# Kernel optimization log

Hardware: AMD Instinct MI355X
Metric: run time of the kernel (lower is better)

## Reference

```python
import jax, jax.numpy as jnp
import numpy as np


def setup_inputs() -> dict:
    key = jax.random.key(0)
    k0, k1, k2, k3, k4, k5 = jax.random.split(key, 6)
    B, V, Fin, K, Fout = 8, 49152, 64, 3, 64
    nnz = V * 8  # ~8 neighbors per vertex (HEALPix sphere graph)
    std = (2.0 / (Fin * K)) ** 0.5  # Kaiming-normal as in reset_parameters
    inputs = jax.random.normal(k0, (B, V, Fin), jnp.float32)
    weight = jax.random.normal(k1, (Fin, K, Fout), jnp.float32) * std
    bias = jax.random.normal(k2, (Fout,), jnp.float32) * 0.05
    lap_rows = jax.random.randint(k3, (nnz,), 0, V, jnp.int32)
    lap_cols = jax.random.randint(k4, (nnz,), 0, V, jnp.int32)
    lap_vals = jax.random.normal(k5, (nnz,), jnp.float32) * 0.1
    return {"inputs": inputs, "weight": weight, "bias": bias,
            "lap_rows": lap_rows, "lap_cols": lap_cols, "lap_vals": lap_vals}


def reference(inputs, weight, bias, lap_rows, lap_cols, lap_vals):
    B, V, Fin = inputs.shape
    _, K, Fout = weight.shape

    def spmm(x):  # sparse Laplacian (COO) @ dense [V, Fin*B]
        return jax.ops.segment_sum(lap_vals[:, None] * x[lap_cols], lap_rows,
                                   num_segments=V)

    # x0: [V, Fin*B], matching torch's permute(1,2,0).view(V, Fin*B)
    x0 = inputs.transpose(1, 2, 0).reshape(V, Fin * B)
    xs = [x0]
    if K > 1:
        x1 = spmm(x0)
        xs.append(x1)
    for _ in range(2, K):
        x2 = 2.0 * spmm(x1) - x0  # Chebyshev recurrence
        xs.append(x2)
        x0, x1 = x1, x2
    x = jnp.stack(xs)                                    # [K, V, Fin*B]
    x = x.reshape(K, V, Fin, B).transpose(3, 1, 2, 0)    # [B, V, Fin, K]
    x = x.reshape(B * V, Fin * K)
    out = x @ weight.reshape(Fin * K, Fout)              # dense GEMM
    return out.reshape(B, V, Fout) + bias
```

## Files before the change

kernel.cpp:

```cpp
#include <hip/hip_runtime.h>
#include <stdint.h>

#define B_   8
#define V_   49152
#define M_   (B_ * V_)

typedef unsigned short ushort_t;
typedef __attribute__((ext_vector_type(8))) short short8;
typedef __attribute__((ext_vector_type(4))) float float4v;

__device__ __forceinline__ float bf2f_lo(unsigned int pk) {
    union { unsigned int u; float f; } x; x.u = pk << 16; return x.f;
}
__device__ __forceinline__ float bf2f_hi(unsigned int pk) {
    union { unsigned int u; float f; } x; x.u = pk & 0xffff0000u; return x.f;
}
__device__ __forceinline__ ushort_t f2bf(float f) {
    union { unsigned int u; float f; } x; x.f = f;
    unsigned int u = x.u;
    unsigned int r = u + 0x7fffu + ((u >> 16) & 1u);
    return (ushort_t)(r >> 16);
}
__device__ __forceinline__ unsigned int pack2(float a, float b) {
    return ((unsigned int)f2bf(b) << 16) | (unsigned int)f2bf(a);
}
__device__ __forceinline__ void fma8(float* acc, float w, const uint4& p) {
    const unsigned int* u = (const unsigned int*)&p;
    #pragma unroll
    for (int i = 0; i < 4; i++) {
        acc[2 * i]     += w * bf2f_lo(u[i]);
        acc[2 * i + 1] += w * bf2f_hi(u[i]);
    }
}

__global__ void fill_sentinel(float* out, int n) {
    int i = blockIdx.x * blockDim.x + threadIdx.x;
    if (i < n) out[i] = 9999.0f;
}

#define PREP_B 3072
__global__ __launch_bounds__(256) void k1_fused(const float* __restrict__ inp,
                                                ushort_t* __restrict__ x0t,
                                                const int* __restrict__ rows, int nnz,
                                                int* __restrict__ counts,
                                                const float* __restrict__ wgt,
                                                ushort_t* __restrict__ wBf, int hb) {
    int bid = blockIdx.x;
    int t = threadIdx.x;
    if (bid < PREP_B) {
        int idx = bid * 256 + t;
        int f4 = idx & 15, v = idx >> 4;
        #pragma unroll
        for (int b = 0; b < 8; b++) {
            float4 d = *(const float4*)(inp + ((size_t)b * V_ + v) * 64 + f4 * 4);
            uint2 o = make_uint2(pack2(d.x, d.y), pack2(d.z, d.w));
            *(uint2*)(x0t + ((size_t)v * 8 + b) * 64 + f4 * 4) = o;
        }
    } else if (bid < PREP_B + hb) {
        int i = (bid - PREP_B) * 256 + t;
        if (i < nnz) atomicAdd(&counts[rows[i]], 1);
    } else {
        int idx = (bid - PREP_B - hb) * 256 + t;
        int j = idx & 7, lane = (idx >> 3) & 63, ntc = (idx >> 9) & 3, kb = idx >> 11;
        int k = kb * 32 + (lane >> 4) * 8 + j;
        int kc = k >> 6, fi = k & 63;
        int fo = ntc * 16 + (lane & 15);
        float w;
        if (kc == 0)      w = wgt[(fi * 3 + 0) * 64 + fo] - wgt[(fi * 3 + 2) * 64 + fo];
        else if (kc == 1) w = wgt[(fi * 3 + 1) * 64 + fo];
        else              w = 2.0f * wgt[(fi * 3 + 2) * 64 + fo];
        wBf[idx] = f2bf(w);
    }
}

__global__ __launch_bounds__(1024) void scan_kernel(const int* __restrict__ counts,
                                                    int* __restrict__ offsets) {
    __shared__ int s[1024];
    int t = threadIdx.x;
    int4 c[12];
    int sum = 0;
    #pragma unroll
    for (int j = 0; j < 12; j++) {
        int4 q = ((const int4*)counts)[t * 12 + j];
        q.x = (q.x + 3) & ~3; q.y = (q.y + 3) & ~3;
        q.z = (q.z + 3) & ~3; q.w = (q.w + 3) & ~3;
        c[j] = q;
        sum += q.x + q.y + q.z + q.w;
    }
    s[t] = sum;
    __syncthreads();
    for (int off = 1; off < 1024; off <<= 1) {
        int v = (t >= off) ? s[t - off] : 0;
        __syncthreads();
        s[t] += v;
        __syncthreads();
    }
    int run = (t == 0) ? 0 : s[t - 1];
    #pragma unroll
    for (int j = 0; j < 12; j++) {
        int4 o;
        o.x = run; run += c[j].x;
        o.y = run; run += c[j].y;
        o.z = run; run += c[j].z;
        o.w = run; run += c[j].w;
        ((int4*)offsets)[t * 12 + j] = o;
    }
    if (t == 1023) offsets[V_] = run;
}

__global__ void bucket_kernel(const int* __restrict__ rows, const int* __restrict__ cols,
                              const float* __restrict__ vals, int nnz,
                              const int* __restrict__ offsets, int* __restrict__ cursor,
                              uint2* __restrict__ e_cv) {
    int i = blockIdx.x * blockDim.x + threadIdx.x;
    if (i >= nnz) return;
    int r = rows[i];
    int p = offsets[r] + atomicAdd(&cursor[r], 1);
    e_cv[p] = make_uint2((unsigned int)cols[i], __float_as_uint(vals[i]));
}

__device__ __forceinline__ void gather16(const ushort_t* __restrict__ srcbf,
                                         const uint2* __restrict__ e_cv,
                                         int beg, int end, float* acc) {
    for (int e = beg; e < end; e += 4) {
        uint4 E0 = *(const uint4*)(e_cv + e);
        uint4 E1 = *(const uint4*)(e_cv + e + 2);
        float w0 = __uint_as_float(E0.y), w1 = __uint_as_float(E0.w);
        float w2 = __uint_as_float(E1.y), w3 = __uint_as_float(E1.w);
        const ushort_t* p0 = srcbf + ((size_t)E0.x * 512);
        const ushort_t* p1 = srcbf + ((size_t)E0.z * 512);
        const ushort_t* p2 = srcbf + ((size_t)E1.x * 512);
        const ushort_t* p3 = srcbf + ((size_t)E1.z * 512);
        uint4 a0 = *(const uint4*)p0, b0 = *(const uint4*)(p0 + 8);
        uint4 a1 = *(const uint4*)p1, b1 = *(const uint4*)(p1 + 8);
        uint4 a2 = *(const uint4*)p2, b2 = *(const uint4*)(p2 + 8);
        uint4 a3 = *(const uint4*)p3, b3 = *(const uint4*)(p3 + 8);
        fma8(acc, w0, a0); fma8(acc + 8, w0, b0);
        fma8(acc, w1, a1); fma8(acc + 8, w1, b1);
        fma8(acc, w2, a2); fma8(acc + 8, w2, b2);
        fma8(acc, w3, a3); fma8(acc + 8, w3, b3);
    }
}

__global__ __launch_bounds__(256) void spmm1_kernel(const ushort_t* __restrict__ x0t,
                                                    const int* __restrict__ offsets,
                                                    const uint2* __restrict__ e_cv,
                                                    ushort_t* __restrict__ x1) {
    int t = threadIdx.x;
    int vi = t >> 5, b = (t >> 2) & 7, f8 = t & 3;
    int v = blockIdx.x * 8 + vi;
    float acc[16];
    #pragma unroll
    for (int i = 0; i < 16; i++) acc[i] = 0.f;
    gather16(x0t + b * 64 + f8 * 16, e_cv, offsets[v], offsets[v + 1], acc);
    unsigned int opk[8];
    #pragma unroll
    for (int i = 0; i < 8; i++) opk[i] = pack2(acc[2 * i], acc[2 * i + 1]);
    ushort_t* dst = x1 + ((size_t)v * 8 + b) * 64 + f8 * 16;
    *(uint4*)dst       = make_uint4(opk[0], opk[1], opk[2], opk[3]);
    *(uint4*)(dst + 8) = make_uint4(opk[4], opk[5], opk[6], opk[7]);
}

__global__ __launch_bounds__(256) void spmm2_gemm(const ushort_t* __restrict__ x0t,
                                                  const ushort_t* __restrict__ x1,
                                                  const int* __restrict__ offsets,
                                                  const uint2* __restrict__ e_cv,
                                                  const ushort_t* __restrict__ wBf,
                                                  const float* __restrict__ bias,
                                                  float* __restrict__ out) {
    __shared__ ushort_t sh[64 * 72];
    int t = threadIdx.x;
    int lane = t & 63, wv = t >> 6;
    int quad = lane >> 4, col = lane & 15;
    int v0 = blockIdx.x * 8;
    int m0 = v0 * 8 + wv * 16;

    size_t arow = (size_t)(m0 + col) * 64 + quad * 8;
    short8 A0[2], A1[2];
    A0[0] = *(const short8*)(x0t + arow);
    A0[1] = *(const short8*)(x0t + arow + 32);
    A1[0] = *(const short8*)(x1 + arow);
    A1[1] = *(const short8*)(x1 + arow + 32);

    int vi = t >> 5, b = (t >> 2) & 7, f8 = t & 3;
    int v = v0 + vi;
    float acc[16];
    #pragma unroll
    for (int i = 0; i < 16; i++) acc[i] = 0.f;
    gather16(x1 + b * 64 + f8 * 16, e_cv, offsets[v], offsets[v + 1], acc);

    unsigned int opk[8];
    #pragma unroll
    for (int i = 0; i < 8; i++) opk[i] = pack2(acc[2 * i], acc[2 * i + 1]);
    int mg = vi * 8 + b;
    ushort_t* dst = sh + mg * 72 + f8 * 16;
    *(uint4*)dst       = make_uint4(opk[0], opk[1], opk[2], opk[3]);
    *(uint4*)(dst + 8) = make_uint4(opk[4], opk[5], opk[6], opk[7]);
    __syncthreads();

    short8 Bf[6][4];
    #pragma unroll
    for (int kb = 0; kb < 6; kb++)
        #pragma unroll
        for (int ntc = 0; ntc < 4; ntc++)
            Bf[kb][ntc] = *(const short8*)(wBf + ((size_t)((kb * 4 + ntc) * 64 + lane)) * 8);

    float bv[4];
    #pragma unroll
    for (int ntc = 0; ntc < 4; ntc++) bv[ntc] = bias[ntc * 16 + col];

    float4v accm[4];
    #pragma unroll
    for (int ntc = 0; ntc < 4; ntc++) accm[ntc] = (float4v){0.f, 0.f, 0.f, 0.f};

    #pragma unroll
    for (int p = 0; p < 2; p++) {
        #pragma unroll
        for (int ntc = 0; ntc < 4; ntc++)
            accm[ntc] = __builtin_amdgcn_mfma_f32_16x16x32_bf16(A0[p], Bf[p][ntc], accm[ntc], 0, 0, 0);
    }
    #pragma unroll
    for (int p = 0; p < 2; p++) {
        #pragma unroll
        for (int ntc = 0; ntc < 4; ntc++)
            accm[ntc] = __builtin_amdgcn_mfma_f32_16x16x32_bf16(A1[p], Bf[2 + p][ntc], accm[ntc], 0, 0, 0);
    }
    #pragma unroll
    for (int p = 0; p < 2; p++) {
        short8 A = *(const short8*)(sh + (wv * 16 + col) * 72 + quad * 8 + p * 32);
        #pragma unroll
        for (int ntc = 0; ntc < 4; ntc++)
            accm[ntc] = __builtin_amdgcn_mfma_f32_16x16x32_bf16(A, Bf[4 + p][ntc], accm[ntc], 0, 0, 0);
    }

    #pragma unroll
    for (int reg = 0; reg < 4; reg++) {
        int m = m0 + quad * 4 + reg;
        int vv = m >> 3, bb = m & 7;
        float* orow = out + ((size_t)bb * V_ + vv) * 64;
        #pragma unroll
        for (int ntc = 0; ntc < 4; ntc++)
            orow[ntc * 16 + col] = accm[ntc][reg] + bv[ntc];
    }
}

extern "C" void kernel_launch(void* const* d_in, const int* in_sizes, int n_in,
                              void* d_out, int out_size, void* d_ws, size_t ws_size,
                              hipStream_t stream) {
    const float* inp  = (const float*)d_in[0];
    const float* wgt  = (const float*)d_in[1];
    const float* bias = (const float*)d_in[2];
    const int*   rows = (const int*)d_in[3];
    const int*   cols = (const int*)d_in[4];
    const float* vals = (const float*)d_in[5];
    int nnz = in_sizes[3];
    float* out = (float*)d_out;
    (void)n_in; (void)out_size;

    char* ws = (char*)d_ws;
    size_t o = 0;
    auto alloc = [&](size_t bytes) { void* p = ws + o; o += (bytes + 255) & ~(size_t)255; return p; };
    size_t meta0 = o;
    int*      counts  = (int*)alloc((size_t)V_ * 4);
    int*      cursor  = (int*)alloc((size_t)V_ * 4);
    int*      offsets = (int*)alloc(((size_t)V_ + 1) * 4);
    size_t nnz_pad = (size_t)nnz + 3 * (size_t)V_;
    uint2*    e_cv    = (uint2*)alloc(nnz_pad * 8);
    size_t meta_bytes = o - meta0;
    ushort_t* x0t     = (ushort_t*)alloc((size_t)M_ * 64 * 2);
    ushort_t* x1      = (ushort_t*)alloc((size_t)M_ * 64 * 2);
    ushort_t* wBf     = (ushort_t*)alloc(6 * 4 * 64 * 8 * 2);

    if (ws_size < o) {
        fill_sentinel<<<(M_ * 64 + 255) / 256, 256, 0, stream>>>(out, M_ * 64);
        return;
    }

    int hb = (nnz + 255) / 256;
    hipMemsetAsync((char*)ws + meta0, 0, meta_bytes, stream);
    k1_fused<<<PREP_B + hb + 48, 256, 0, stream>>>(inp, x0t, rows, nnz, counts, wgt, wBf, hb);
    scan_kernel<<<1, 1024, 0, stream>>>(counts, offsets);
    bucket_kernel<<<hb, 256, 0, stream>>>(rows, cols, vals, nnz, offsets, cursor, e_cv);
    spmm1_kernel<<<V_ / 8, 256, 0, stream>>>(x0t, offsets, e_cv, x1);
    spmm2_gemm<<<V_ / 8, 256, 0, stream>>>(x0t, x1, offsets, e_cv, wBf, bias, out);
}
```

Measured before the change: 368.8 us.

## Replace CSR build with fixed-capacity per-row edge buckets and unroll gather

Drops the count, scan and bucket passes. Edges are now written directly into per-row slots of fixed capacity 48 using an atomic cursor inside the fused prep kernel, which removes two kernel launches and one pass over the COO arrays. The SpMM kernels read the row length from the cursor and pad it to a multiple of 8, relying on zeroed slots so the padding adds nothing. The gather loop is also unrolled from 4 to 8 edges to keep more loads in flight. In exchange, the memset grows to cover a larger edge buffer, and any row with more than 48 nonzeros would have its extra edges silently dropped.

```diff
diff --git a/kernel.cpp b/kernel.cpp
--- a/kernel.cpp
+++ b/kernel.cpp
@@ -4,6 +4,7 @@
 #define B_   8
 #define V_   49152
 #define M_   (B_ * V_)
+#define CAP_ 48
 
 typedef unsigned short ushort_t;
 typedef __attribute__((ext_vector_type(8))) short short8;
@@ -41,10 +42,13 @@
 #define PREP_B 3072
 __global__ __launch_bounds__(256) void k1_fused(const float* __restrict__ inp,
                                                 ushort_t* __restrict__ x0t,
-                                                const int* __restrict__ rows, int nnz,
-                                                int* __restrict__ counts,
+                                                const int* __restrict__ rows,
+                                                const int* __restrict__ cols,
+                                                const float* __restrict__ vals, int nnz,
+                                                int* __restrict__ cursor,
+                                                uint2* __restrict__ e_cv,
                                                 const float* __restrict__ wgt,
-                                                ushort_t* __restrict__ wBf, int hb) {
+                                                ushort_t* __restrict__ wBf) {
     int bid = blockIdx.x;
     int t = threadIdx.x;
     if (bid < PREP_B) {
@@ -56,11 +60,8 @@
             uint2 o = make_uint2(pack2(d.x, d.y), pack2(d.z, d.w));
             *(uint2*)(x0t + ((size_t)v * 8 + b) * 64 + f4 * 4) = o;
         }
-    } else if (bid < PREP_B + hb) {
-        int i = (bid - PREP_B) * 256 + t;
-        if (i < nnz) atomicAdd(&counts[rows[i]], 1);
-    } else {
-        int idx = (bid - PREP_B - hb) * 256 + t;
+    } else if (bid < PREP_B + 48) {
+        int idx = (bid - PREP_B) * 256 + t;
         int j = idx & 7, lane = (idx >> 3) & 63, ntc = (idx >> 9) & 3, kb = idx >> 11;
         int k = kb * 32 + (lane >> 4) * 8 + j;
         int kc = k >> 6, fi = k & 63;
@@ -70,89 +71,70 @@
         else if (kc == 1) w = wgt[(fi * 3 + 1) * 64 + fo];
         else              w = 2.0f * wgt[(fi * 3 + 2) * 64 + fo];
         wBf[idx] = f2bf(w);
-    }
-}
-
-__global__ __launch_bounds__(1024) void scan_kernel(const int* __restrict__ counts,
-                                                    int* __restrict__ offsets) {
-    __shared__ int s[1024];
-    int t = threadIdx.x;
-    int4 c[12];
-    int sum = 0;
-    #pragma unroll
-    for (int j = 0; j < 12; j++) {
-        int4 q = ((const int4*)counts)[t * 12 + j];
-        q.x = (q.x + 3) & ~3; q.y = (q.y + 3) & ~3;
-        q.z = (q.z + 3) & ~3; q.w = (q.w + 3) & ~3;
-        c[j] = q;
-        sum += q.x + q.y + q.z + q.w;
-    }
-    s[t] = sum;
-    __syncthreads();
-    for (int off = 1; off < 1024; off <<= 1) {
-        int v = (t >= off) ? s[t - off] : 0;
-        __syncthreads();
-        s[t] += v;
-        __syncthreads();
-    }
-    int run = (t == 0) ? 0 : s[t - 1];
-    #pragma unroll
-    for (int j = 0; j < 12; j++) {
-        int4 o;
-        o.x = run; run += c[j].x;
-        o.y = run; run += c[j].y;
-        o.z = run; run += c[j].z;
-        o.w = run; run += c[j].w;
-        ((int4*)offsets)[t * 12 + j] = o;
-    }
-    if (t == 1023) offsets[V_] = run;
-}
-
-__global__ void bucket_kernel(const int* __restrict__ rows, const int* __restrict__ cols,
-                              const float* __restrict__ vals, int nnz,
-                              const int* __restrict__ offsets, int* __restrict__ cursor,
-                              uint2* __restrict__ e_cv) {
-    int i = blockIdx.x * blockDim.x + threadIdx.x;
-    if (i >= nnz) return;
-    int r = rows[i];
-    int p = offsets[r] + atomicAdd(&cursor[r], 1);
-    e_cv[p] = make_uint2((unsigned int)cols[i], __float_as_uint(vals[i]));
+    } else {
+        int i = (bid - PREP_B - 48) * 256 + t;
+        if (i < nnz) {
+            int r = rows[i];
+            int pos = atomicAdd(&cursor[r], 1);
+            if (pos < CAP_)
+                e_cv[(size_t)r * CAP_ + pos] = make_uint2((unsigned int)cols[i],
+                                                          __float_as_uint(vals[i]));
+        }
+    }
 }
 
 __device__ __forceinline__ void gather16(const ushort_t* __restrict__ srcbf,
                                          const uint2* __restrict__ e_cv,
                                          int beg, int end, float* acc) {
-    for (int e = beg; e < end; e += 4) {
+    for (int e = beg; e < end; e += 8) {
         uint4 E0 = *(const uint4*)(e_cv + e);
         uint4 E1 = *(const uint4*)(e_cv + e + 2);
-        float w0 = __uint_as_float(E0.y), w1 = __uint_as_float(E0.w);
-        float w2 = __uint_as_float(E1.y), w3 = __uint_as_float(E1.w);
+        uint4 E2 = *(const uint4*)(e_cv + e + 4);
+        uint4 E3 = *(const uint4*)(e_cv + e + 6);
         const ushort_t* p0 = srcbf + ((size_t)E0.x * 512);
         const ushort_t* p1 = srcbf + ((size_t)E0.z * 512);
         const ushort_t* p2 = srcbf + ((size_t)E1.x * 512);
         const ushort_t* p3 = srcbf + ((size_t)E1.z * 512);
+        const ushort_t* p4 = srcbf + ((size_t)E2.x * 512);
+        const ushort_t* p5 = srcbf + ((size_t)E2.z * 512);
+        const ushort_t* p6 = srcbf + ((size_t)E3.x * 512);
+        const ushort_t* p7 = srcbf + ((size_t)E3.z * 512);
         uint4 a0 = *(const uint4*)p0, b0 = *(const uint4*)(p0 + 8);
         uint4 a1 = *(const uint4*)p1, b1 = *(const uint4*)(p1 + 8);
         uint4 a2 = *(const uint4*)p2, b2 = *(const uint4*)(p2 + 8);
         uint4 a3 = *(const uint4*)p3, b3 = *(const uint4*)(p3 + 8);
+        uint4 a4 = *(const uint4*)p4, b4 = *(const uint4*)(p4 + 8);
+        uint4 a5 = *(const uint4*)p5, b5 = *(const uint4*)(p5 + 8);
+        uint4 a6 = *(const uint4*)p6, b6 = *(const uint4*)(p6 + 8);
+        uint4 a7 = *(const uint4*)p7, b7 = *(const uint4*)(p7 + 8);
+        float w0 = __uint_as_float(E0.y), w1 = __uint_as_float(E0.w);
+        float w2 = __uint_as_float(E1.y), w3 = __uint_as_float(E1.w);
+        float w4 = __uint_as_float(E2.y), w5 = __uint_as_float(E2.w);
+        float w6 = __uint_as_float(E3.y), w7 = __uint_as_float(E3.w);
         fma8(acc, w0, a0); fma8(acc + 8, w0, b0);
         fma8(acc, w1, a1); fma8(acc + 8, w1, b1);
         fma8(acc, w2, a2); fma8(acc + 8, w2, b2);
         fma8(acc, w3, a3); fma8(acc + 8, w3, b3);
+        fma8(acc, w4, a4); fma8(acc + 8, w4, b4);
+        fma8(acc, w5, a5); fma8(acc + 8, w5, b5);
+        fma8(acc, w6, a6); fma8(acc + 8, w6, b6);
+        fma8(acc, w7, a7); fma8(acc + 8, w7, b7);
     }
 }
 
 __global__ __launch_bounds__(256) void spmm1_kernel(const ushort_t* __restrict__ x0t,
-                                                    const int* __restrict__ offsets,
+                                                    const int* __restrict__ cursor,
                                                     const uint2* __restrict__ e_cv,
                                                     ushort_t* __restrict__ x1) {
     int t = threadIdx.x;
     int vi = t >> 5, b = (t >> 2) & 7, f8 = t & 3;
     int v = blockIdx.x * 8 + vi;
+    int beg = v * CAP_;
+    int end = beg + ((cursor[v] + 7) & ~7);
     float acc[16];
     #pragma unroll
     for (int i = 0; i < 16; i++) acc[i] = 0.f;
-    gather16(x0t + b * 64 + f8 * 16, e_cv, offsets[v], offsets[v + 1], acc);
+    gather16(x0t + b * 64 + f8 * 16, e_cv, beg, end, acc);
     unsigned int opk[8];
     #pragma unroll
     for (int i = 0; i < 8; i++) opk[i] = pack2(acc[2 * i], acc[2 * i + 1]);
@@ -163,7 +145,7 @@
 
 __global__ __launch_bounds__(256) void spmm2_gemm(const ushort_t* __restrict__ x0t,
                                                   const ushort_t* __restrict__ x1,
-                                                  const int* __restrict__ offsets,
+                                                  const int* __restrict__ cursor,
                                                   const uint2* __restrict__ e_cv,
                                                   const ushort_t* __restrict__ wBf,
                                                   const float* __restrict__ bias,
@@ -184,10 +166,12 @@
 
     int vi = t >> 5, b = (t >> 2) & 7, f8 = t & 3;
     int v = v0 + vi;
+    int beg = v * CAP_;
+    int end = beg + ((cursor[v] + 7) & ~7);
     float acc[16];
     #pragma unroll
     for (int i = 0; i < 16; i++) acc[i] = 0.f;
-    gather16(x1 + b * 64 + f8 * 16, e_cv, offsets[v], offsets[v + 1], acc);
+    gather16(x1 + b * 64 + f8 * 16, e_cv, beg, end, acc);
 
     unsigned int opk[8];
     #pragma unroll
@@ -261,15 +245,12 @@
     size_t o = 0;
     auto alloc = [&](size_t bytes) { void* p = ws + o; o += (bytes + 255) & ~(size_t)255; return p; };
     size_t meta0 = o;
-    int*      counts  = (int*)alloc((size_t)V_ * 4);
-    int*      cursor  = (int*)alloc((size_t)V_ * 4);
-    int*      offsets = (int*)alloc(((size_t)V_ + 1) * 4);
-    size_t nnz_pad = (size_t)nnz + 3 * (size_t)V_;
-    uint2*    e_cv    = (uint2*)alloc(nnz_pad * 8);
+    int*      cursor = (int*)alloc((size_t)V_ * 4);
+    uint2*    e_cv   = (uint2*)alloc((size_t)V_ * CAP_ * 8);
     size_t meta_bytes = o - meta0;
-    ushort_t* x0t     = (ushort_t*)alloc((size_t)M_ * 64 * 2);
-    ushort_t* x1      = (ushort_t*)alloc((size_t)M_ * 64 * 2);
-    ushort_t* wBf     = (ushort_t*)alloc(6 * 4 * 64 * 8 * 2);
+    ushort_t* x0t    = (ushort_t*)alloc((size_t)M_ * 64 * 2);
+    ushort_t* x1     = (ushort_t*)alloc((size_t)M_ * 64 * 2);
+    ushort_t* wBf    = (ushort_t*)alloc(6 * 4 * 64 * 8 * 2);
 
     if (ws_size < o) {
         fill_sentinel<<<(M_ * 64 + 255) / 256, 256, 0, stream>>>(out, M_ * 64);
@@ -278,9 +259,8 @@
 
     int hb = (nnz + 255) / 256;
     hipMemsetAsync((char*)ws + meta0, 0, meta_bytes, stream);
-    k1_fused<<<PREP_B + hb + 48, 256, 0, stream>>>(inp, x0t, rows, nnz, counts, wgt, wBf, hb);
-    scan_kernel<<<1, 1024, 0, stream>>>(counts, offsets);
-    bucket_kernel<<<hb, 256, 0, stream>>>(rows, cols, vals, nnz, offsets, cursor, e_cv);
-    spmm1_kernel<<<V_ / 8, 256, 0, stream>>>(x0t, offsets, e_cv, x1);
-    spmm2_gemm<<<V_ / 8, 256, 0, stream>>>(x0t, x1, offsets, e_cv, wBf, bias, out);
-}
+    k1_fused<<<PREP_B + 48 + hb, 256, 0, stream>>>(inp, x0t, rows, cols, vals, nnz,
+                                                   cursor, e_cv, wgt, wBf);
+    spmm1_kernel<<<V_ / 8, 256, 0, stream>>>(x0t, cursor, e_cv, x1);
+    spmm2_gemm<<<V_ / 8, 256, 0, stream>>>(x0t, x1, cursor, e_cv, wBf, bias, out);
+}
```

Measured after the change: 352.1 us. 4.5% less time.
